# Kernel optimization log

Hardware: AMD Instinct MI355X
Metric: run time of the kernel (lower is better)

Reference implementation:

```python
import jax, jax.numpy as jnp
import numpy as np

LOW_DIM, SKIP_DIM, OUT_DIM = 512, 256, 256
EPS_IDW = 1e-8
EPS_LN = 1e-5
K = 3


def setup_inputs() -> dict:
    key = jax.random.key(0)
    ks = jax.random.split(key, 10)
    B, N, S = 4, 8192, 2048
    xyz_hi = jax.random.uniform(ks[0], (B, N, 3), dtype=jnp.float32)
    xyz_lo = jax.random.uniform(ks[1], (B, S, 3), dtype=jnp.float32)
    feat_skip = jax.random.normal(ks[2], (B, N, SKIP_DIM), dtype=jnp.float32)
    feat_lo = jax.random.normal(ks[3], (B, S, LOW_DIM), dtype=jnp.float32)
    in_dim = LOW_DIM + SKIP_DIM
    W1 = jax.random.normal(ks[4], (in_dim, OUT_DIM), dtype=jnp.float32) / np.sqrt(in_dim)
    b1 = jnp.zeros((OUT_DIM,), dtype=jnp.float32)
    W2 = jax.random.normal(ks[5], (OUT_DIM, OUT_DIM), dtype=jnp.float32) / np.sqrt(OUT_DIM)
    b2 = jnp.zeros((OUT_DIM,), dtype=jnp.float32)
    gamma = jnp.ones((OUT_DIM,), dtype=jnp.float32)
    beta = jnp.zeros((OUT_DIM,), dtype=jnp.float32)
    return {"xyz_hi": xyz_hi, "xyz_lo": xyz_lo, "feat_skip": feat_skip,
            "feat_lo": feat_lo, "W1": W1, "b1": b1, "W2": W2, "b2": b2,
            "gamma": gamma, "beta": beta}


def _layer_norm(x, gamma, beta):
    mu = jnp.mean(x, axis=-1, keepdims=True)
    var = jnp.mean(jnp.square(x - mu), axis=-1, keepdims=True)
    return (x - mu) * jax.lax.rsqrt(var + EPS_LN) * gamma + beta


def reference(xyz_hi, xyz_lo, feat_skip, feat_lo, W1, b1, W2, b2, gamma, beta):
    B, N, _ = xyz_hi.shape
    _, S, _ = xyz_lo.shape
    if S == 1:
        interpolated = jnp.broadcast_to(feat_lo, (B, N, feat_lo.shape[-1]))
    else:
        # pairwise Euclidean distances: (B, N, S)
        d2 = (jnp.sum(xyz_hi ** 2, -1)[:, :, None]
              + jnp.sum(xyz_lo ** 2, -1)[:, None, :]
              - 2.0 * jnp.einsum('bnd,bsd->bns', xyz_hi, xyz_lo))
        dists = jnp.sqrt(jnp.maximum(d2, 0.0))
        # smallest-3 via top_k on negated distances
        neg_d, knn_idx = jax.lax.top_k(-dists, K)          # (B, N, 3)
        dk = -neg_d
        inv_d = 1.0 / (dk + EPS_IDW)
        weights = inv_d / jnp.sum(inv_d, axis=-1, keepdims=True)  # (B, N, 3)
        # gather neighbor features: (B, N, 3, low_dim)
        knn_feat = feat_lo[jnp.arange(B)[:, None, None], knn_idx]
        interpolated = jnp.einsum('bnk,bnkc->bnc', weights, knn_feat)
    fused = jnp.concatenate([feat_skip, interpolated], axis=-1)   # (B, N, skip+low)
    h = jax.nn.relu(fused @ W1 + b1)
    h = h @ W2 + b2
    return _layer_norm(h, gamma, beta)
```

## Files before the change

kernel.cpp:

```cpp
#include <hip/hip_runtime.h>
#include <hip/hip_bf16.h>
#include <stdint.h>

typedef unsigned short u16;
typedef __attribute__((ext_vector_type(8))) short short8;
typedef __attribute__((ext_vector_type(4))) float f32x4;

#define BB 4
#define NN 8192
#define SS 2048
#define MTOT 32768
#define CSKIP 256
#define CLO 512
#define CIN 768
#define COUT 256

__device__ __forceinline__ u16 f2bf(float f) {
  unsigned u = __float_as_uint(f);
  u += 0x7fffu + ((u >> 16) & 1u);
  return (u16)(u >> 16);
}

__device__ __forceinline__ void gl_lds16(const void* g, void* l) {
  __builtin_amdgcn_global_load_lds(
      (const __attribute__((address_space(1))) void*)g,
      (__attribute__((address_space(3))) void*)l, 16, 0, 0);
}

__global__ __launch_bounds__(512) void knn_wconv_kernel(
    const float* __restrict__ xyz_hi, const float* __restrict__ xyz_lo,
    const float* __restrict__ W1, const float* __restrict__ W2,
    float* __restrict__ wq_g, int* __restrict__ iq_g,
    u16* __restrict__ W1aT, u16* __restrict__ W1bT, u16* __restrict__ W2T) {
  int blk = blockIdx.x;
  if (blk >= 512) {
    int base = (blk - 512) * 512 + threadIdx.x;
    for (int i = base; i < 262144; i += 65536) {
      if (i < 65536) {
        int n = i >> 8, k = i & 255;
        W1aT[i] = f2bf(W1[(size_t)k * COUT + n]);
      } else if (i < 196608) {
        int j = i - 65536;
        int n = j >> 9, k = j & 511;
        W1bT[j] = f2bf(W1[(size_t)(256 + k) * COUT + n]);
      } else {
        int j = i - 196608;
        int n = j >> 8, k = j & 255;
        W2T[j] = f2bf(W2[(size_t)k * COUT + n]);
      }
    }
    return;
  }

  __shared__ float4 sxyz[SS];
  __shared__ float md[8][64][3];
  __shared__ int   mi[8][64][3];

  int tid = threadIdx.x;
  int b = blk >> 7;
  const float* xl = xyz_lo + (size_t)b * SS * 3;
  for (int j = tid; j < SS; j += 512)
    sxyz[j] = make_float4(xl[j * 3 + 0], xl[j * 3 + 1], xl[j * 3 + 2], 0.f);
  __syncthreads();

  int wave = tid >> 6, lane = tid & 63;
  int qm = blk * 64 + lane;
  float qx = xyz_hi[(size_t)qm * 3 + 0];
  float qy = xyz_hi[(size_t)qm * 3 + 1];
  float qz = xyz_hi[(size_t)qm * 3 + 2];

  float b0 = 1e30f, b1 = 1e30f, b2 = 1e30f;
  int i0 = -1, i1 = -1, i2 = -1;
  int j0 = wave * 256;
#pragma unroll 4
  for (int jj = 0; jj < 256; ++jj) {
    int j = j0 + jj;
    float4 p = sxyz[j];
    float dx = p.x - qx, dy = p.y - qy, dz = p.z - qz;
    float d = fmaf(dx, dx, fmaf(dy, dy, dz * dz));
    if (d < b2) {
      bool c0 = d < b0, c1 = d < b1;
      float nb0 = fminf(b0, d);
      float nb1 = __builtin_amdgcn_fmed3f(b0, b1, d);
      float nb2 = c1 ? b1 : d;
      i2 = c1 ? i1 : j;
      i1 = c0 ? i0 : (c1 ? j : i1);
      i0 = c0 ? j : i0;
      b0 = nb0; b1 = nb1; b2 = nb2;
    }
  }
  md[wave][lane][0] = b0; mi[wave][lane][0] = i0;
  md[wave][lane][1] = b1; mi[wave][lane][1] = i1;
  md[wave][lane][2] = b2; mi[wave][lane][2] = i2;
  __syncthreads();

  if (tid < 64) {
    int q = tid;
    float fb0 = 1e30f, fb1 = 1e30f, fb2 = 1e30f;
    int fi0 = -1, fi1 = -1, fi2 = -1;
    for (int p = 0; p < 8; ++p)
#pragma unroll
      for (int s = 0; s < 3; ++s) {
        float d = md[p][q][s]; int ix = mi[p][q][s];
        if (d < fb2 || (d == fb2 && ix < fi2)) {
          fb2 = d; fi2 = ix;
          if (fb2 < fb1 || (fb2 == fb1 && fi2 < fi1)) {
            float t = fb1; fb1 = fb2; fb2 = t; int ti = fi1; fi1 = fi2; fi2 = ti;
          }
          if (fb1 < fb0 || (fb1 == fb0 && fi1 < fi0)) {
            float t = fb0; fb0 = fb1; fb1 = t; int ti = fi0; fi0 = fi1; fi1 = ti;
          }
        }
      }
    int qm2 = blk * 64 + q;
    float d0 = sqrtf(fb0), d1 = sqrtf(fb1), d2 = sqrtf(fb2);
    float inv0 = 1.0f / (d0 + 1e-8f);
    float inv1 = 1.0f / (d1 + 1e-8f);
    float inv2 = 1.0f / (d2 + 1e-8f);
    float s = inv0 + inv1 + inv2;
    wq_g[(size_t)qm2 * 3 + 0] = inv0 / s;
    wq_g[(size_t)qm2 * 3 + 1] = inv1 / s;
    wq_g[(size_t)qm2 * 3 + 2] = inv2 / s;
    iq_g[(size_t)qm2 * 3 + 0] = fi0;
    iq_g[(size_t)qm2 * 3 + 1] = fi1;
    iq_g[(size_t)qm2 * 3 + 2] = fi2;
  }
}

__global__ __launch_bounds__(256, 4) void ggemm_kernel(
    const float* __restrict__ feat_lo, const u16* __restrict__ W1bT,
    float* __restrict__ G) {
  __shared__ u16 As[32 * 40];
  __shared__ u16 Bs[256 * 32];
  int tid = threadIdx.x;
  int m0 = blockIdx.x << 5;
  int w = tid >> 6, lane = tid & 63;
  int quad = lane >> 4, l16 = lane & 15;

  int srow = tid >> 3, s4 = (tid & 7) << 2;
  const float* arow = feat_lo + (size_t)(m0 + srow) * CLO + s4;
  u16* As_dst = As + srow * 40 + s4;

  f32x4 zero = {0.f, 0.f, 0.f, 0.f};
  f32x4 acc[2][4];
#pragma unroll
  for (int tm = 0; tm < 2; ++tm)
#pragma unroll
    for (int tn = 0; tn < 4; ++tn) acc[tm][tn] = zero;

  for (int kc = 0; kc < 16; ++kc) {
    __syncthreads();
#pragma unroll
    for (int r = 0; r < 4; ++r) {
      int u = tid + r * 256;
      int nrow = u >> 2, c = u & 3;
      int cg = c ^ (nrow & 3);
      gl_lds16(W1bT + (size_t)nrow * CLO + kc * 32 + cg * 8, (char*)Bs + u * 16);
    }
    float4 av = *(const float4*)(arow + kc * 32);
    union { __hip_bfloat162 h2[2]; uint2 u2; } pk;
    pk.h2[0] = __float22bfloat162_rn(make_float2(av.x, av.y));
    pk.h2[1] = __float22bfloat162_rn(make_float2(av.z, av.w));
    *(uint2*)As_dst = pk.u2;
    __syncthreads();

    short8 af[2], bf[4];
#pragma unroll
    for (int t = 0; t < 2; ++t)
      af[t] = *(const short8*)(As + (t * 16 + l16) * 40 + quad * 8);
#pragma unroll
    for (int t = 0; t < 4; ++t) {
      int rr = w * 64 + t * 16 + l16;
      bf[t] = *(const short8*)(Bs + (rr * 4 + (quad ^ (rr & 3))) * 8);
    }
#pragma unroll
    for (int tm = 0; tm < 2; ++tm)
#pragma unroll
      for (int tn = 0; tn < 4; ++tn)
        acc[tm][tn] = __builtin_amdgcn_mfma_f32_16x16x32_bf16(af[tm], bf[tn], acc[tm][tn], 0, 0, 0);
  }

#pragma unroll
  for (int tm = 0; tm < 2; ++tm)
#pragma unroll
    for (int tn = 0; tn < 4; ++tn) {
      int col = w * 64 + tn * 16 + l16;
#pragma unroll
      for (int r = 0; r < 4; ++r) {
        int row = m0 + tm * 16 + quad * 4 + r;
        G[(size_t)row * COUT + col] = acc[tm][tn][r];
      }
    }
}

__global__ __launch_bounds__(256, 2) void gemm12_kernel(
    const float* __restrict__ feat_skip, const u16* __restrict__ W1aT,
    const float* __restrict__ b1, const float* __restrict__ G,
    const float* __restrict__ wq_g, const int* __restrict__ iq_g,
    const u16* __restrict__ W2T, const float* __restrict__ b2,
    const float* __restrict__ gamma, const float* __restrict__ beta,
    float* __restrict__ out) {
  __shared__ u16 Hs[64 * 264];
  __shared__ u16 Bs[256 * 32];
  __shared__ u16 As[64 * 40];
  __shared__ float swq[192];
  __shared__ int   siq[192];
  __shared__ float red[4][64][2];
  __shared__ float stats[64][2];
  int tid = threadIdx.x;
  int m0 = blockIdx.x << 6;
  int bS = (m0 >> 13) * SS;
  int w = tid >> 6, lane = tid & 63;
  int quad = lane >> 4, l16 = lane & 15;

  if (tid < 192) {
    swq[tid] = wq_g[(size_t)m0 * 3 + tid];
    siq[tid] = iq_g[(size_t)m0 * 3 + tid];
  }

  int srow = tid >> 2, sc8 = (tid & 3) << 3;
  const float* arow = feat_skip + (size_t)(m0 + srow) * CSKIP + sc8;
  u16* As_dst = As + srow * 40 + sc8;

  f32x4 zero = {0.f, 0.f, 0.f, 0.f};
  f32x4 acc[4][4];
#pragma unroll
  for (int tm = 0; tm < 4; ++tm)
#pragma unroll
    for (int tn = 0; tn < 4; ++tn) acc[tm][tn] = zero;

  for (int kc = 0; kc < 8; ++kc) {
    __syncthreads();
#pragma unroll
    for (int r = 0; r < 4; ++r) {
      int u = tid + r * 256;
      int nrow = u >> 2, c = u & 3;
      int cg = c ^ (nrow & 3);
      gl_lds16(W1aT + (size_t)nrow * CSKIP + kc * 32 + cg * 8, (char*)Bs + u * 16);
    }
    float4 x0 = *(const float4*)(arow + kc * 32);
    float4 x1 = *(const float4*)(arow + kc * 32 + 4);
    union { __hip_bfloat162 h2[4]; uint4 u4; } pk;
    pk.h2[0] = __float22bfloat162_rn(make_float2(x0.x, x0.y));
    pk.h2[1] = __float22bfloat162_rn(make_float2(x0.z, x0.w));
    pk.h2[2] = __float22bfloat162_rn(make_float2(x1.x, x1.y));
    pk.h2[3] = __float22bfloat162_rn(make_float2(x1.z, x1.w));
    *(uint4*)As_dst = pk.u4;
    __syncthreads();

    short8 af[4], bf[4];
#pragma unroll
    for (int t = 0; t < 4; ++t)
      af[t] = *(const short8*)(As + (t * 16 + l16) * 40 + quad * 8);
#pragma unroll
    for (int t = 0; t < 4; ++t) {
      int rr = w * 64 + t * 16 + l16;
      bf[t] = *(const short8*)(Bs + (rr * 4 + (quad ^ (rr & 3))) * 8);
    }
#pragma unroll
    for (int tm = 0; tm < 4; ++tm)
#pragma unroll
      for (int tn = 0; tn < 4; ++tn)
        acc[tm][tn] = __builtin_amdgcn_mfma_f32_16x16x32_bf16(af[tm], bf[tn], acc[tm][tn], 0, 0, 0);
  }

  {
    float bias[4];
#pragma unroll
    for (int tn = 0; tn < 4; ++tn) bias[tn] = b1[w * 64 + tn * 16 + l16];
#pragma unroll
    for (int tm = 0; tm < 4; ++tm)
#pragma unroll
      for (int r = 0; r < 4; ++r) {
        int rl = tm * 16 + quad * 4 + r;
        float w0 = swq[rl * 3 + 0], w1 = swq[rl * 3 + 1], w2 = swq[rl * 3 + 2];
        const float* g0 = G + (size_t)(bS + siq[rl * 3 + 0]) * COUT;
        const float* g1 = G + (size_t)(bS + siq[rl * 3 + 1]) * COUT;
        const float* g2 = G + (size_t)(bS + siq[rl * 3 + 2]) * COUT;
#pragma unroll
        for (int tn = 0; tn < 4; ++tn) {
          int col = w * 64 + tn * 16 + l16;
          float gv = fmaf(w0, g0[col], fmaf(w1, g1[col], w2 * g2[col]));
          float v = acc[tm][tn][r] + bias[tn] + gv;
          v = v > 0.f ? v : 0.f;
          Hs[rl * 264 + col] = f2bf(v);
        }
      }
  }

#pragma unroll
  for (int tm = 0; tm < 4; ++tm)
#pragma unroll
    for (int tn = 0; tn < 4; ++tn) acc[tm][tn] = zero;

  for (int kc = 0; kc < 8; ++kc) {
    __syncthreads();
#pragma unroll
    for (int r = 0; r < 4; ++r) {
      int u = tid + r * 256;
      int nrow = u >> 2, c = u & 3;
      int cg = c ^ (nrow & 3);
      gl_lds16(W2T + (size_t)nrow * COUT + kc * 32 + cg * 8, (char*)Bs + u * 16);
    }
    __syncthreads();

    short8 af[4], bf[4];
#pragma unroll
    for (int t = 0; t < 4; ++t)
      af[t] = *(const short8*)(Hs + (t * 16 + l16) * 264 + kc * 32 + quad * 8);
#pragma unroll
    for (int t = 0; t < 4; ++t) {
      int rr = w * 64 + t * 16 + l16;
      bf[t] = *(const short8*)(Bs + (rr * 4 + (quad ^ (rr & 3))) * 8);
    }
#pragma unroll
    for (int tm = 0; tm < 4; ++tm)
#pragma unroll
      for (int tn = 0; tn < 4; ++tn)
        acc[tm][tn] = __builtin_amdgcn_mfma_f32_16x16x32_bf16(af[tm], bf[tn], acc[tm][tn], 0, 0, 0);
  }

  float bias[4], g[4], be[4];
#pragma unroll
  for (int tn = 0; tn < 4; ++tn) {
    int col = w * 64 + tn * 16 + l16;
    bias[tn] = b2[col]; g[tn] = gamma[col]; be[tn] = beta[col];
  }
#pragma unroll
  for (int tm = 0; tm < 4; ++tm)
#pragma unroll
    for (int r = 0; r < 4; ++r) {
      float s = 0.f, sq = 0.f;
#pragma unroll
      for (int tn = 0; tn < 4; ++tn) {
        float v = acc[tm][tn][r] + bias[tn];
        acc[tm][tn][r] = v;
        s += v; sq += v * v;
      }
#pragma unroll
      for (int msk = 1; msk < 16; msk <<= 1) {
        s += __shfl_xor(s, msk);
        sq += __shfl_xor(sq, msk);
      }
      if (l16 == 0) {
        int rl = tm * 16 + quad * 4 + r;
        red[w][rl][0] = s;
        red[w][rl][1] = sq;
      }
    }
  __syncthreads();
  if (tid < 64) {
    float s = red[0][tid][0] + red[1][tid][0] + red[2][tid][0] + red[3][tid][0];
    float sq = red[0][tid][1] + red[1][tid][1] + red[2][tid][1] + red[3][tid][1];
    float mu = s * (1.f / 256.f);
    float var = sq * (1.f / 256.f) - mu * mu;
    stats[tid][0] = mu;
    stats[tid][1] = rsqrtf(var + 1e-5f);
  }
  __syncthreads();
#pragma unroll
  for (int tm = 0; tm < 4; ++tm)
#pragma unroll
    for (int r = 0; r < 4; ++r) {
      int rl = tm * 16 + quad * 4 + r;
      float mu = stats[rl][0], rstd = stats[rl][1];
#pragma unroll
      for (int tn = 0; tn < 4; ++tn) {
        int col = w * 64 + tn * 16 + l16;
        out[(size_t)(m0 + rl) * COUT + col] = (acc[tm][tn][r] - mu) * rstd * g[tn] + be[tn];
      }
    }
}

extern "C" void kernel_launch(void* const* d_in, const int* in_sizes, int n_in,
                              void* d_out, int out_size, void* d_ws, size_t ws_size,
                              hipStream_t stream) {
  const float* xyz_hi    = (const float*)d_in[0];
  const float* xyz_lo    = (const float*)d_in[1];
  const float* feat_skip = (const float*)d_in[2];
  const float* feat_lo   = (const float*)d_in[3];
  const float* W1        = (const float*)d_in[4];
  const float* b1        = (const float*)d_in[5];
  const float* W2        = (const float*)d_in[6];
  const float* b2        = (const float*)d_in[7];
  const float* gamma     = (const float*)d_in[8];
  const float* beta      = (const float*)d_in[9];
  float* out = (float*)d_out;

  char* ws = (char*)d_ws;
  u16*   W1aT  = (u16*)(ws + 16777216);
  u16*   W1bT  = (u16*)(ws + 16908288);
  u16*   W2T   = (u16*)(ws + 17170432);
  float* wq_g  = (float*)(ws + 17301504);
  int*   iq_g  = (int*)(ws + 17694720);
  float* G     = (float*)(ws + 18087936);

  knn_wconv_kernel<<<640, 512, 0, stream>>>(xyz_hi, xyz_lo, W1, W2,
                                            wq_g, iq_g, W1aT, W1bT, W2T);
  ggemm_kernel<<<(BB * SS) / 32, 256, 0, stream>>>(feat_lo, W1bT, G);
  gemm12_kernel<<<MTOT / 64, 256, 0, stream>>>(feat_skip, W1aT, b1, G, wq_g, iq_g,
                                               W2T, b2, gamma, beta, out);
}
```

Baseline: 185.9 us.

## Split KNN from weight conversion, stream candidates via wave-uniform global loads, branchless top-3

Weight conversion and packing of xyz_lo into float4 move into a separate prep kernel. The KNN kernel then reads candidate points from global memory with a wave-uniform index (readfirstlane) instead of staging them in LDS, which should let the compiler use scalar loads and drops the LDS fill and barrier. The top-3 insertion becomes branchless using med3, and the unroll factor rises to 8. The cost is an extra kernel launch and a top-3 update that now runs for every candidate instead of only when one qualifies.

Result: no change. 182.3 us (-1.9%).

```diff
diff --git a/kernel.cpp b/kernel.cpp
--- a/kernel.cpp
+++ b/kernel.cpp
@@ -27,67 +27,67 @@
       (__attribute__((address_space(3))) void*)l, 16, 0, 0);
 }
 
-__global__ __launch_bounds__(512) void knn_wconv_kernel(
-    const float* __restrict__ xyz_hi, const float* __restrict__ xyz_lo,
-    const float* __restrict__ W1, const float* __restrict__ W2,
-    float* __restrict__ wq_g, int* __restrict__ iq_g,
-    u16* __restrict__ W1aT, u16* __restrict__ W1bT, u16* __restrict__ W2T) {
-  int blk = blockIdx.x;
-  if (blk >= 512) {
-    int base = (blk - 512) * 512 + threadIdx.x;
-    for (int i = base; i < 262144; i += 65536) {
-      if (i < 65536) {
-        int n = i >> 8, k = i & 255;
-        W1aT[i] = f2bf(W1[(size_t)k * COUT + n]);
-      } else if (i < 196608) {
-        int j = i - 65536;
-        int n = j >> 9, k = j & 511;
-        W1bT[j] = f2bf(W1[(size_t)(256 + k) * COUT + n]);
-      } else {
-        int j = i - 196608;
-        int n = j >> 8, k = j & 255;
-        W2T[j] = f2bf(W2[(size_t)k * COUT + n]);
-      }
-    }
-    return;
-  }
-
-  __shared__ float4 sxyz[SS];
+__global__ __launch_bounds__(256) void wconv_kernel(const float* __restrict__ W1,
+                                                    const float* __restrict__ W2,
+                                                    const float* __restrict__ xyz_lo,
+                                                    u16* __restrict__ W1aT,
+                                                    u16* __restrict__ W1bT,
+                                                    u16* __restrict__ W2T,
+                                                    float4* __restrict__ sxyz_g) {
+  int i = blockIdx.x * 256 + threadIdx.x;
+  if (i < 65536) {
+    int n = i >> 8, k = i & 255;
+    W1aT[i] = f2bf(W1[(size_t)k * COUT + n]);
+  } else if (i < 196608) {
+    int j = i - 65536;
+    int n = j >> 9, k = j & 511;
+    W1bT[j] = f2bf(W1[(size_t)(256 + k) * COUT + n]);
+  } else if (i < 262144) {
+    int j = i - 196608;
+    int n = j >> 8, k = j & 255;
+    W2T[j] = f2bf(W2[(size_t)k * COUT + n]);
+  } else if (i < 262144 + BB * SS) {
+    int j = i - 262144;
+    sxyz_g[j] = make_float4(xyz_lo[j * 3 + 0], xyz_lo[j * 3 + 1],
+                            xyz_lo[j * 3 + 2], 0.f);
+  }
+}
+
+__global__ __launch_bounds__(512) void knn_kernel(
+    const float* __restrict__ xyz_hi, const float4* __restrict__ sxyz_g,
+    float* __restrict__ wq_g, int* __restrict__ iq_g) {
   __shared__ float md[8][64][3];
   __shared__ int   mi[8][64][3];
 
   int tid = threadIdx.x;
+  int blk = blockIdx.x;
   int b = blk >> 7;
-  const float* xl = xyz_lo + (size_t)b * SS * 3;
-  for (int j = tid; j < SS; j += 512)
-    sxyz[j] = make_float4(xl[j * 3 + 0], xl[j * 3 + 1], xl[j * 3 + 2], 0.f);
-  __syncthreads();
-
   int wave = tid >> 6, lane = tid & 63;
   int qm = blk * 64 + lane;
   float qx = xyz_hi[(size_t)qm * 3 + 0];
   float qy = xyz_hi[(size_t)qm * 3 + 1];
   float qz = xyz_hi[(size_t)qm * 3 + 2];
 
+  const float4* cand = sxyz_g + b * SS;
+  int j0 = __builtin_amdgcn_readfirstlane(wave * 256);
+
   float b0 = 1e30f, b1 = 1e30f, b2 = 1e30f;
   int i0 = -1, i1 = -1, i2 = -1;
-  int j0 = wave * 256;
-#pragma unroll 4
+#pragma unroll 8
   for (int jj = 0; jj < 256; ++jj) {
     int j = j0 + jj;
-    float4 p = sxyz[j];
+    float4 p = cand[j];
     float dx = p.x - qx, dy = p.y - qy, dz = p.z - qz;
     float d = fmaf(dx, dx, fmaf(dy, dy, dz * dz));
-    if (d < b2) {
-      bool c0 = d < b0, c1 = d < b1;
-      float nb0 = fminf(b0, d);
-      float nb1 = __builtin_amdgcn_fmed3f(b0, b1, d);
-      float nb2 = c1 ? b1 : d;
-      i2 = c1 ? i1 : j;
-      i1 = c0 ? i0 : (c1 ? j : i1);
-      i0 = c0 ? j : i0;
-      b0 = nb0; b1 = nb1; b2 = nb2;
-    }
+    bool c0 = d < b0, c1 = d < b1, c2 = d < b2;
+    float nb0 = fminf(b0, d);
+    float nb1 = __builtin_amdgcn_fmed3f(b0, b1, d);
+    float nb2 = __builtin_amdgcn_fmed3f(b1, b2, d);
+    int ni0 = c0 ? j : i0;
+    int ni1 = c0 ? i0 : (c1 ? j : i1);
+    int ni2 = c1 ? i1 : (c2 ? j : i2);
+    b0 = nb0; b1 = nb1; b2 = nb2;
+    i0 = ni0; i1 = ni1; i2 = ni2;
   }
   md[wave][lane][0] = b0; mi[wave][lane][0] = i0;
   md[wave][lane][1] = b1; mi[wave][lane][1] = i1;
@@ -388,15 +388,16 @@
   float* out = (float*)d_out;
 
   char* ws = (char*)d_ws;
-  u16*   W1aT  = (u16*)(ws + 16777216);
-  u16*   W1bT  = (u16*)(ws + 16908288);
-  u16*   W2T   = (u16*)(ws + 17170432);
-  float* wq_g  = (float*)(ws + 17301504);
-  int*   iq_g  = (int*)(ws + 17694720);
-  float* G     = (float*)(ws + 18087936);
-
-  knn_wconv_kernel<<<640, 512, 0, stream>>>(xyz_hi, xyz_lo, W1, W2,
-                                            wq_g, iq_g, W1aT, W1bT, W2T);
+  u16*    W1aT   = (u16*)(ws + 16777216);
+  u16*    W1bT   = (u16*)(ws + 16908288);
+  u16*    W2T    = (u16*)(ws + 17170432);
+  float*  wq_g   = (float*)(ws + 17301504);
+  int*    iq_g   = (int*)(ws + 17694720);
+  float*  G      = (float*)(ws + 18087936);
+  float4* sxyz_g = (float4*)(ws + 26476544);
+
+  wconv_kernel<<<1056, 256, 0, stream>>>(W1, W2, xyz_lo, W1aT, W1bT, W2T, sxyz_g);
+  knn_kernel<<<MTOT / 64, 512, 0, stream>>>(xyz_hi, sxyz_g, wq_g, iq_g);
   ggemm_kernel<<<(BB * SS) / 32, 256, 0, stream>>>(feat_lo, W1bT, G);
   gemm12_kernel<<<MTOT / 64, 256, 0, stream>>>(feat_skip, W1aT, b1, G, wq_g, iq_g,
                                                W2T, b2, gamma, beta, out);
```

## Widen KNN blocks to 16 waves, drop LDS staging, double-buffer W2 tiles

Applied to the files above, without the earlier changes.

The KNN kernel now runs 1024-thread blocks with 16 waves each scanning 128 candidates. Candidate coordinates are read straight from global memory at wave-uniform addresses instead of being staged in LDS, and the per-candidate update is branchless using med3. The launch grid drops to 576 blocks, and the weight-conversion blocks handle 1024 elements each. In the fused GEMM kernel the W2 tiles are double-buffered, so the next tile's global-to-LDS load is issued before the current tile's MFMAs, which removes one barrier per iteration. Risks: scalar/global load latency in the KNN loop, always doing the select work, and the extra LDS buffer lowering occupancy.

Result: faster. 178.9 us (-3.8%).

```diff
diff --git a/kernel.cpp b/kernel.cpp
--- a/kernel.cpp
+++ b/kernel.cpp
@@ -27,14 +27,15 @@
       (__attribute__((address_space(3))) void*)l, 16, 0, 0);
 }
 
-__global__ __launch_bounds__(512) void knn_wconv_kernel(
+__global__ __launch_bounds__(1024) void knn_wconv_kernel(
     const float* __restrict__ xyz_hi, const float* __restrict__ xyz_lo,
     const float* __restrict__ W1, const float* __restrict__ W2,
     float* __restrict__ wq_g, int* __restrict__ iq_g,
     u16* __restrict__ W1aT, u16* __restrict__ W1bT, u16* __restrict__ W2T) {
   int blk = blockIdx.x;
+  int tid = threadIdx.x;
   if (blk >= 512) {
-    int base = (blk - 512) * 512 + threadIdx.x;
+    int base = (blk - 512) * 1024 + tid;
     for (int i = base; i < 262144; i += 65536) {
       if (i < 65536) {
         int n = i >> 8, k = i & 255;
@@ -52,42 +53,38 @@
     return;
   }
 
-  __shared__ float4 sxyz[SS];
-  __shared__ float md[8][64][3];
-  __shared__ int   mi[8][64][3];
-
-  int tid = threadIdx.x;
+  __shared__ float md[16][64][3];
+  __shared__ int   mi[16][64][3];
+
   int b = blk >> 7;
-  const float* xl = xyz_lo + (size_t)b * SS * 3;
-  for (int j = tid; j < SS; j += 512)
-    sxyz[j] = make_float4(xl[j * 3 + 0], xl[j * 3 + 1], xl[j * 3 + 2], 0.f);
-  __syncthreads();
-
   int wave = tid >> 6, lane = tid & 63;
   int qm = blk * 64 + lane;
   float qx = xyz_hi[(size_t)qm * 3 + 0];
   float qy = xyz_hi[(size_t)qm * 3 + 1];
   float qz = xyz_hi[(size_t)qm * 3 + 2];
 
+  const float* xl = xyz_lo + (size_t)b * SS * 3;
+  int j0 = __builtin_amdgcn_readfirstlane(wave * 128);
+
   float b0 = 1e30f, b1 = 1e30f, b2 = 1e30f;
   int i0 = -1, i1 = -1, i2 = -1;
-  int j0 = wave * 256;
-#pragma unroll 4
-  for (int jj = 0; jj < 256; ++jj) {
+#pragma unroll 8
+  for (int jj = 0; jj < 128; ++jj) {
     int j = j0 + jj;
-    float4 p = sxyz[j];
-    float dx = p.x - qx, dy = p.y - qy, dz = p.z - qz;
+    float px = xl[3 * j + 0];
+    float py = xl[3 * j + 1];
+    float pz = xl[3 * j + 2];
+    float dx = px - qx, dy = py - qy, dz = pz - qz;
     float d = fmaf(dx, dx, fmaf(dy, dy, dz * dz));
-    if (d < b2) {
-      bool c0 = d < b0, c1 = d < b1;
-      float nb0 = fminf(b0, d);
-      float nb1 = __builtin_amdgcn_fmed3f(b0, b1, d);
-      float nb2 = c1 ? b1 : d;
-      i2 = c1 ? i1 : j;
-      i1 = c0 ? i0 : (c1 ? j : i1);
-      i0 = c0 ? j : i0;
-      b0 = nb0; b1 = nb1; b2 = nb2;
-    }
+    bool c0 = d < b0, c1 = d < b1, c2 = d < b2;
+    float nb0 = fminf(b0, d);
+    float nb1 = __builtin_amdgcn_fmed3f(b0, b1, d);
+    float nb2 = __builtin_amdgcn_fmed3f(b1, b2, d);
+    int ni0 = c0 ? j : i0;
+    int ni1 = c0 ? i0 : (c1 ? j : i1);
+    int ni2 = c1 ? i1 : (c2 ? j : i2);
+    b0 = nb0; b1 = nb1; b2 = nb2;
+    i0 = ni0; i1 = ni1; i2 = ni2;
   }
   md[wave][lane][0] = b0; mi[wave][lane][0] = i0;
   md[wave][lane][1] = b1; mi[wave][lane][1] = i1;
@@ -98,7 +95,7 @@
     int q = tid;
     float fb0 = 1e30f, fb1 = 1e30f, fb2 = 1e30f;
     int fi0 = -1, fi1 = -1, fi2 = -1;
-    for (int p = 0; p < 8; ++p)
+    for (int p = 0; p < 16; ++p)
 #pragma unroll
       for (int s = 0; s < 3; ++s) {
         float d = md[p][q][s]; int ix = mi[p][q][s];
@@ -202,6 +199,7 @@
     float* __restrict__ out) {
   __shared__ u16 Hs[64 * 264];
   __shared__ u16 Bs[256 * 32];
+  __shared__ u16 Bs2[256 * 32];
   __shared__ u16 As[64 * 40];
   __shared__ float swq[192];
   __shared__ int   siq[192];
@@ -293,17 +291,28 @@
 #pragma unroll
     for (int tn = 0; tn < 4; ++tn) acc[tm][tn] = zero;
 
+  __syncthreads();
+#pragma unroll
+  for (int r = 0; r < 4; ++r) {
+    int u = tid + r * 256;
+    int nrow = u >> 2, c = u & 3;
+    int cg = c ^ (nrow & 3);
+    gl_lds16(W2T + (size_t)nrow * COUT + cg * 8, (char*)Bs + u * 16);
+  }
   for (int kc = 0; kc < 8; ++kc) {
     __syncthreads();
-#pragma unroll
-    for (int r = 0; r < 4; ++r) {
-      int u = tid + r * 256;
-      int nrow = u >> 2, c = u & 3;
-      int cg = c ^ (nrow & 3);
-      gl_lds16(W2T + (size_t)nrow * COUT + kc * 32 + cg * 8, (char*)Bs + u * 16);
-    }
-    __syncthreads();
-
+    u16* cur = (kc & 1) ? Bs2 : Bs;
+    u16* nxt = (kc & 1) ? Bs : Bs2;
+    if (kc + 1 < 8) {
+#pragma unroll
+      for (int r = 0; r < 4; ++r) {
+        int u = tid + r * 256;
+        int nrow = u >> 2, c = u & 3;
+        int cg = c ^ (nrow & 3);
+        gl_lds16(W2T + (size_t)nrow * COUT + (kc + 1) * 32 + cg * 8,
+                 (char*)nxt + u * 16);
+      }
+    }
     short8 af[4], bf[4];
 #pragma unroll
     for (int t = 0; t < 4; ++t)
@@ -311,7 +320,7 @@
 #pragma unroll
     for (int t = 0; t < 4; ++t) {
       int rr = w * 64 + t * 16 + l16;
-      bf[t] = *(const short8*)(Bs + (rr * 4 + (quad ^ (rr & 3))) * 8);
+      bf[t] = *(const short8*)(cur + (rr * 4 + (quad ^ (rr & 3))) * 8);
     }
 #pragma unroll
     for (int tm = 0; tm < 4; ++tm)
@@ -395,8 +404,8 @@
   int*   iq_g  = (int*)(ws + 17694720);
   float* G     = (float*)(ws + 18087936);
 
-  knn_wconv_kernel<<<640, 512, 0, stream>>>(xyz_hi, xyz_lo, W1, W2,
-                                            wq_g, iq_g, W1aT, W1bT, W2T);
+  knn_wconv_kernel<<<576, 1024, 0, stream>>>(xyz_hi, xyz_lo, W1, W2,
+                                             wq_g, iq_g, W1aT, W1bT, W2T);
   ggemm_kernel<<<(BB * SS) / 32, 256, 0, stream>>>(feat_lo, W1bT, G);
   gemm12_kernel<<<MTOT / 64, 256, 0, stream>>>(feat_skip, W1aT, b1, G, wq_g, iq_g,
                                                W2T, b2, gamma, beta, out);
```
